# Kernel optimization log

Hardware: AMD Instinct MI355X
Metric: run time of the kernel (lower is better)

Reference implementation:

```python
import jax, jax.numpy as jnp
import numpy as np

EMBEDDINGS = 16
DENSE = 256
HEAD_SIZE = 64


def setup_inputs() -> dict:
    key = jax.random.key(0)
    ks = jax.random.split(key, 7)
    B, T = 4096, 100
    x = jax.random.normal(ks[0], (B, T, EMBEDDINGS), dtype=jnp.float32)
    s1 = EMBEDDINGS ** -0.5
    s2 = HEAD_SIZE ** -0.5
    # Linear weights stored as [in, out] (torch stores transposed; math identical)
    Wk = jax.random.uniform(ks[1], (EMBEDDINGS, HEAD_SIZE), jnp.float32, -s1, s1)
    Wq = jax.random.uniform(ks[2], (EMBEDDINGS, HEAD_SIZE), jnp.float32, -s1, s1)
    Wv = jax.random.uniform(ks[3], (EMBEDDINGS, HEAD_SIZE), jnp.float32, -s1, s1)
    Wdk = jax.random.uniform(ks[4], (HEAD_SIZE, DENSE), jnp.float32, -s2, s2)
    Wdq = jax.random.uniform(ks[5], (HEAD_SIZE, DENSE), jnp.float32, -s2, s2)
    Wdv = jax.random.uniform(ks[6], (HEAD_SIZE, DENSE), jnp.float32, -s2, s2)
    return {"x": x, "Wk": Wk, "Wq": Wq, "Wv": Wv, "Wdk": Wdk, "Wdq": Wdq, "Wdv": Wdv}


def reference(x, Wk, Wq, Wv, Wdk, Wdq, Wdv):
    B, T, C = x.shape
    # two chained bias-free projections per stream: [B,T,C] -> [B,T,H] -> [B,T,DENSE]
    k = (x @ Wk) @ Wdk
    q = (x @ Wq) @ Wdq
    v = (x @ Wv) @ Wdv
    # NOTE: original scales by C**-0.5 where C is the INPUT embedding dim (16)
    wei = jnp.einsum("btd,bsd->bts", q, k) * (C ** -0.5)  # [B,T,T]
    causal = jnp.tril(jnp.ones((T, T), dtype=bool))
    wei = jnp.where(causal, wei, -jnp.inf)
    wei = jax.nn.softmax(wei, axis=-1)
    # dropout omitted (eval-mode reference; training dropout is stochastic)
    out = wei @ v  # [B,T,DENSE]
    return out
```

## Files before the change

### kernel.cpp

```cpp
#include <hip/hip_runtime.h>

#define T_SEQ 100
#define C_EMB 16
#define DCOL  256


__global__ __launch_bounds__(256) void prep_kernel(
    const float* __restrict__ Wk, const float* __restrict__ Wq,
    const float* __restrict__ Wv, const float* __restrict__ Wdk,
    const float* __restrict__ Wdq, const float* __restrict__ Wdv,
    float* __restrict__ ws)
{
    __shared__ float WQL[16][260];
    __shared__ float WKL[16][260];
    const int tid = threadIdx.x;

    float aq[16], ak[16], av[16];
    #pragma unroll
    for (int i = 0; i < 16; ++i) { aq[i] = 0.f; ak[i] = 0.f; av[i] = 0.f; }
    for (int h = 0; h < 64; ++h) {
        const float wdq = Wdq[h*256 + tid];
        const float wdk = Wdk[h*256 + tid];
        const float wdv = Wdv[h*256 + tid];
        #pragma unroll
        for (int i = 0; i < 16; ++i) {
            aq[i] += Wq[i*64 + h] * wdq;
            ak[i] += Wk[i*64 + h] * wdk;
            av[i] += Wv[i*64 + h] * wdv;
        }
    }
    #pragma unroll
    for (int i = 0; i < 16; ++i) {
        WQL[i][tid] = aq[i];
        WKL[i][tid] = ak[i];
        ws[256 + i*256 + tid] = av[i];
    }
    __syncthreads();

    {
        const float scale = 0.25f * 1.4426950408889634f;
        const int k = tid >> 4;
        const int c = tid & 15;
        float acc = 0.f;
        for (int d4 = 0; d4 < 64; ++d4) {
            float4 a = *(const float4*)&WQL[k][4*d4];
            float4 b = *(const float4*)&WKL[c][4*d4];
            acc += a.x*b.x + a.y*b.y + a.z*b.z + a.w*b.w;
        }
        ws[k*16 + c] = acc * scale;
    }
}

__global__ __launch_bounds__(128) void attn_z_kernel(
    const float* __restrict__ x, const float* __restrict__ ws,
    float* __restrict__ Z, const int zstride)
{
    const int b   = blockIdx.x;
    const int tid = threadIdx.x;
    const int t   = tid;
    const int wid = tid >> 6;

    const float* __restrict__ xb = x + (size_t)b * (T_SEQ * C_EMB);

    const int tl = (t < T_SEQ) ? t : (T_SEQ - 1);
    float xt[16];
    #pragma unroll
    for (int i = 0; i < 4; ++i) {
        float4 q = ((const float4*)(xb + tl * 16))[i];
        xt[4*i+0] = q.x; xt[4*i+1] = q.y; xt[4*i+2] = q.z; xt[4*i+3] = q.w;
    }

    float y[16];
    #pragma unroll
    for (int c = 0; c < 16; ++c) y[c] = 0.f;
    #pragma unroll
    for (int k = 0; k < 16; ++k) {
        const float xk = xt[k];
        #pragma unroll
        for (int c = 0; c < 16; ++c)
            y[c] = fmaf(xk, ws[k*16 + c], y[c]);
    }

    float4 z0 = {0,0,0,0}, z1 = {0,0,0,0}, z2 = {0,0,0,0}, z3 = {0,0,0,0};
    float l = 0.f;

    const int smax = (wid == 0) ? 64 : T_SEQ;
    const float4* __restrict__ X4 = (const float4*)xb;
    #pragma unroll 2
    for (int s = 0; s < smax; ++s) {
        float4 a0 = X4[s*4+0];
        float4 a1 = X4[s*4+1];
        float4 a2 = X4[s*4+2];
        float4 a3 = X4[s*4+3];
        float p0 = fmaf(y[ 3], a0.w, fmaf(y[ 2], a0.z, fmaf(y[ 1], a0.y, y[ 0]*a0.x)));
        float p1 = fmaf(y[ 7], a1.w, fmaf(y[ 6], a1.z, fmaf(y[ 5], a1.y, y[ 4]*a1.x)));
        float p2 = fmaf(y[11], a2.w, fmaf(y[10], a2.z, fmaf(y[ 9], a2.y, y[ 8]*a2.x)));
        float p3 = fmaf(y[15], a3.w, fmaf(y[14], a3.z, fmaf(y[13], a3.y, y[12]*a3.x)));
        float sc = (p0 + p1) + (p2 + p3);
        float p = __builtin_amdgcn_exp2f(sc);
        p = (s <= t) ? p : 0.f;
        l += p;
        z0.x = fmaf(p, a0.x, z0.x); z0.y = fmaf(p, a0.y, z0.y);
        z0.z = fmaf(p, a0.z, z0.z); z0.w = fmaf(p, a0.w, z0.w);
        z1.x = fmaf(p, a1.x, z1.x); z1.y = fmaf(p, a1.y, z1.y);
        z1.z = fmaf(p, a1.z, z1.z); z1.w = fmaf(p, a1.w, z1.w);
        z2.x = fmaf(p, a2.x, z2.x); z2.y = fmaf(p, a2.y, z2.y);
        z2.z = fmaf(p, a2.z, z2.z); z2.w = fmaf(p, a2.w, z2.w);
        z3.x = fmaf(p, a3.x, z3.x); z3.y = fmaf(p, a3.y, z3.y);
        z3.z = fmaf(p, a3.z, z3.z); z3.w = fmaf(p, a3.w, z3.w);
    }

    if (t < T_SEQ) {
        const float li = __builtin_amdgcn_rcpf(l);
        float* __restrict__ zo = Z + ((size_t)b * T_SEQ + t) * zstride;
        float4 o0 = {z0.x*li, z0.y*li, z0.z*li, z0.w*li};
        float4 o1 = {z1.x*li, z1.y*li, z1.z*li, z1.w*li};
        float4 o2 = {z2.x*li, z2.y*li, z2.z*li, z2.w*li};
        float4 o3 = {z3.x*li, z3.y*li, z3.z*li, z3.w*li};
        ((float4*)zo)[0] = o0; ((float4*)zo)[1] = o1;
        ((float4*)zo)[2] = o2; ((float4*)zo)[3] = o3;
    }
}

__global__ __launch_bounds__(256) void out_kernel(
    const float* __restrict__ Z, const int zstride,
    const float* __restrict__ ws, float* __restrict__ out, const int nrows)
{
    const int lane = threadIdx.x & 63;
    const int gw   = (blockIdx.x << 2) + (threadIdx.x >> 6);
    const int nw   = gridDim.x << 2;

    const float* __restrict__ WVp = ws + 256;
    float4 wv[16];
    #pragma unroll
    for (int c = 0; c < 16; ++c)
        wv[c] = *(const float4*)&WVp[c*256 + 4*lane];

    for (int r = gw; r < nrows; r += nw) {
        const int ru = __builtin_amdgcn_readfirstlane(r);
        const float* __restrict__ zr = Z + (size_t)ru * zstride;
        float4 acc = {0.f, 0.f, 0.f, 0.f};
        #pragma unroll
        for (int c = 0; c < 16; ++c) {
            const float zc = zr[c];
            acc.x = fmaf(zc, wv[c].x, acc.x);
            acc.y = fmaf(zc, wv[c].y, acc.y);
            acc.z = fmaf(zc, wv[c].z, acc.z);
            acc.w = fmaf(zc, wv[c].w, acc.w);
        }
        *(float4*)&out[(size_t)ru * DCOL + 4*lane] = acc;
    }
}

extern "C" void kernel_launch(void* const* d_in, const int* in_sizes, int n_in,
                              void* d_out, int out_size, void* d_ws, size_t ws_size,
                              hipStream_t stream) {
    const float* x   = (const float*)d_in[0];
    const float* Wk  = (const float*)d_in[1];
    const float* Wq  = (const float*)d_in[2];
    const float* Wv  = (const float*)d_in[3];
    const float* Wdk = (const float*)d_in[4];
    const float* Wdq = (const float*)d_in[5];
    const float* Wdv = (const float*)d_in[6];
    float* out = (float*)d_out;
    float* ws  = (float*)d_ws;

    const int B     = in_sizes[0] / (T_SEQ * C_EMB);
    const int nrows = B * T_SEQ;

    prep_kernel<<<1, 256, 0, stream>>>(Wk, Wq, Wv, Wdk, Wdq, Wdv, ws);

    const size_t zoff_floats  = 4352;
    const size_t zneed_bytes  = (zoff_floats + (size_t)nrows * 16) * sizeof(float);
    float* Z;
    int zstride;
    if (ws_size >= zneed_bytes) { Z = ws + zoff_floats; zstride = 16;   }
    else                        { Z = out;              zstride = DCOL; }

    attn_z_kernel<<<B, 128, 0, stream>>>(x, ws, Z, zstride);

    out_kernel<<<4096, 256, 0, stream>>>(Z, zstride, ws, out, nrows);
}
```

Before: 557.5 us.

## Split each query row across two lanes in attention-Z kernel

The attention kernel now uses 256 threads per batch, with two lanes per query row. Each lane handles 8 of the 16 channels, and the partial scores are combined with a lane shuffle. Causal loop bounds are set per wave (32, 64, 96 or 100 keys), which cuts the wasted masked iterations that the 64/100 split caused. The change halves per-thread registers and serial work and raises occupancy. In exchange it adds a cross-lane shuffle on every key and duplicates the exp and mask work across the two lanes.

```diff
diff --git a/kernel.cpp b/kernel.cpp
--- a/kernel.cpp
+++ b/kernel.cpp
@@ -51,52 +51,51 @@
     }
 }
 
-__global__ __launch_bounds__(128) void attn_z_kernel(
+__global__ __launch_bounds__(256, 8) void attn_z_kernel(
     const float* __restrict__ x, const float* __restrict__ ws,
     float* __restrict__ Z, const int zstride)
 {
     const int b   = blockIdx.x;
     const int tid = threadIdx.x;
-    const int t   = tid;
-    const int wid = tid >> 6;
+    const int t   = tid >> 1;
+    const int h   = tid & 1;
+    const int wv  = tid >> 6;
 
     const float* __restrict__ xb = x + (size_t)b * (T_SEQ * C_EMB);
+    const int tl = (t < T_SEQ) ? t : (T_SEQ - 1);
 
-    const int tl = (t < T_SEQ) ? t : (T_SEQ - 1);
     float xt[16];
     #pragma unroll
     for (int i = 0; i < 4; ++i) {
         float4 q = ((const float4*)(xb + tl * 16))[i];
         xt[4*i+0] = q.x; xt[4*i+1] = q.y; xt[4*i+2] = q.z; xt[4*i+3] = q.w;
     }
-
-    float y[16];
+    float y[8];
     #pragma unroll
-    for (int c = 0; c < 16; ++c) y[c] = 0.f;
+    for (int c = 0; c < 8; ++c) y[c] = 0.f;
     #pragma unroll
     for (int k = 0; k < 16; ++k) {
         const float xk = xt[k];
-        #pragma unroll
-        for (int c = 0; c < 16; ++c)
-            y[c] = fmaf(xk, ws[k*16 + c], y[c]);
+        float4 m0 = *(const float4*)(ws + k*16 + 8*h);
+        float4 m1 = *(const float4*)(ws + k*16 + 8*h + 4);
+        y[0] = fmaf(xk, m0.x, y[0]); y[1] = fmaf(xk, m0.y, y[1]);
+        y[2] = fmaf(xk, m0.z, y[2]); y[3] = fmaf(xk, m0.w, y[3]);
+        y[4] = fmaf(xk, m1.x, y[4]); y[5] = fmaf(xk, m1.y, y[5]);
+        y[6] = fmaf(xk, m1.z, y[6]); y[7] = fmaf(xk, m1.w, y[7]);
     }
 
-    float4 z0 = {0,0,0,0}, z1 = {0,0,0,0}, z2 = {0,0,0,0}, z3 = {0,0,0,0};
+    float4 z0 = {0,0,0,0}, z1 = {0,0,0,0};
     float l = 0.f;
 
-    const int smax = (wid == 0) ? 64 : T_SEQ;
-    const float4* __restrict__ X4 = (const float4*)xb;
+    const int smax = (wv == 3) ? T_SEQ : 32*(wv + 1);
     #pragma unroll 2
     for (int s = 0; s < smax; ++s) {
-        float4 a0 = X4[s*4+0];
-        float4 a1 = X4[s*4+1];
-        float4 a2 = X4[s*4+2];
-        float4 a3 = X4[s*4+3];
-        float p0 = fmaf(y[ 3], a0.w, fmaf(y[ 2], a0.z, fmaf(y[ 1], a0.y, y[ 0]*a0.x)));
-        float p1 = fmaf(y[ 7], a1.w, fmaf(y[ 6], a1.z, fmaf(y[ 5], a1.y, y[ 4]*a1.x)));
-        float p2 = fmaf(y[11], a2.w, fmaf(y[10], a2.z, fmaf(y[ 9], a2.y, y[ 8]*a2.x)));
-        float p3 = fmaf(y[15], a3.w, fmaf(y[14], a3.z, fmaf(y[13], a3.y, y[12]*a3.x)));
-        float sc = (p0 + p1) + (p2 + p3);
+        float4 a0 = *(const float4*)(xb + s*16 + 8*h);
+        float4 a1 = *(const float4*)(xb + s*16 + 8*h + 4);
+        float part = fmaf(y[3], a0.w, fmaf(y[2], a0.z, fmaf(y[1], a0.y, y[0]*a0.x)));
+        float pb   = fmaf(y[7], a1.w, fmaf(y[6], a1.z, fmaf(y[5], a1.y, y[4]*a1.x)));
+        part += pb;
+        float sc = part + __shfl_xor(part, 1, 64);
         float p = __builtin_amdgcn_exp2f(sc);
         p = (s <= t) ? p : 0.f;
         l += p;
@@ -104,21 +103,15 @@
         z0.z = fmaf(p, a0.z, z0.z); z0.w = fmaf(p, a0.w, z0.w);
         z1.x = fmaf(p, a1.x, z1.x); z1.y = fmaf(p, a1.y, z1.y);
         z1.z = fmaf(p, a1.z, z1.z); z1.w = fmaf(p, a1.w, z1.w);
-        z2.x = fmaf(p, a2.x, z2.x); z2.y = fmaf(p, a2.y, z2.y);
-        z2.z = fmaf(p, a2.z, z2.z); z2.w = fmaf(p, a2.w, z2.w);
-        z3.x = fmaf(p, a3.x, z3.x); z3.y = fmaf(p, a3.y, z3.y);
-        z3.z = fmaf(p, a3.z, z3.z); z3.w = fmaf(p, a3.w, z3.w);
     }
 
     if (t < T_SEQ) {
         const float li = __builtin_amdgcn_rcpf(l);
-        float* __restrict__ zo = Z + ((size_t)b * T_SEQ + t) * zstride;
+        float* __restrict__ zo = Z + ((size_t)b * T_SEQ + t) * zstride + 8*h;
         float4 o0 = {z0.x*li, z0.y*li, z0.z*li, z0.w*li};
         float4 o1 = {z1.x*li, z1.y*li, z1.z*li, z1.w*li};
-        float4 o2 = {z2.x*li, z2.y*li, z2.z*li, z2.w*li};
-        float4 o3 = {z3.x*li, z3.y*li, z3.z*li, z3.w*li};
-        ((float4*)zo)[0] = o0; ((float4*)zo)[1] = o1;
-        ((float4*)zo)[2] = o2; ((float4*)zo)[3] = o3;
+        ((float4*)zo)[0] = o0;
+        ((float4*)zo)[1] = o1;
     }
 }
 
@@ -177,7 +170,7 @@
     if (ws_size >= zneed_bytes) { Z = ws + zoff_floats; zstride = 16;   }
     else                        { Z = out;              zstride = DCOL; }
 
-    attn_z_kernel<<<B, 128, 0, stream>>>(x, ws, Z, zstride);
+    attn_z_kernel<<<B, 256, 0, stream>>>(x, ws, Z, zstride);
 
     out_kernel<<<4096, 256, 0, stream>>>(Z, zstride, ws, out, nrows);
 }
```

After: 606.6 us. +8.8%, slower.
